# Performance work log

Hardware: AMD Instinct MI355X
Metric: run time of the kernel (lower is better)

Reference implementation:

```python
import jax, jax.numpy as jnp
import numpy as np

LAM = 0.01        # self.lam
K_POINTS = 256    # max diagram points kept for matching


def _diagram0(img):
    """0-dim sublevel-set cubical persistence of a 2D image (V-construction,
    4-connectivity) via Kruskal-style union-find over value-sorted pixels.
    Returns (births, deaths, valid) each of shape [H*W]; essential class gets
    death = max(img). Pairs with zero persistence are masked out (as gudhi does)."""
    H, W = img.shape
    N = H * W
    v = img.reshape(-1)
    order = jnp.argsort(v)          # stable ascending filtration order
    rank = jnp.argsort(order)       # rank[i] = position of pixel i in filtration
    idx = jnp.arange(N)
    rows, cols = idx // W, idx % W
    nbr = jnp.stack([
        jnp.where(rows > 0, idx - W, -1),
        jnp.where(rows < H - 1, idx + W, -1),
        jnp.where(cols > 0, idx - 1, -1),
        jnp.where(cols < W - 1, idx + 1, -1)], axis=1)  # [N,4]

    def find(parent, i):
        # root chase with path halving
        def cond(c):
            p, j = c
            return p[j] != j
        def body(c):
            p, j = c
            pj = p[j]
            return p.at[j].set(p[pj]), pj
        p, r = jax.lax.while_loop(cond, body, (parent, i))
        return p, r

    def step(t, carry):
        parent, death = carry
        p = order[t]  # pixel entering the filtration
        def merge(k, carry2):
            parent, death = carry2
            q = nbr[p, k]
            active = (q >= 0) & (rank[jnp.maximum(q, 0)] < t)
            qs = jnp.where(active, jnp.maximum(q, 0), p)
            parent, rp = find(parent, p)
            parent, rq = find(parent, qs)
            do = active & (rp != rq)
            older = jnp.where(rank[rp] < rank[rq], rp, rq)   # smaller birth survives
            young = jnp.where(rank[rp] < rank[rq], rq, rp)   # younger component dies at v[p]
            parent = parent.at[young].set(jnp.where(do, older, parent[young]))
            death = death.at[young].set(jnp.where(do, p, death[young]))
            return parent, death
        return jax.lax.fori_loop(0, 4, merge, (parent, death))

    parent, death = jax.lax.fori_loop(
        0, N, step, (jnp.arange(N), jnp.full((N,), -1, jnp.int32)))
    births = v
    deaths = jnp.where(death >= 0, v[jnp.maximum(death, 0)], jnp.max(v))
    valid = (deaths - births) > 0
    return births, deaths, valid


def _wdist(b1, d1, m1, b2, d2, m2):
    """2-Wasserstein distance between diagrams, approximated by matching the
    top-K points of each diagram sorted by persistence; unmatched points are
    projected to the diagonal (cost pers^2/2). Final (sum cost)^(1/2) (p=2)."""
    def topk(b, d, m):
        pers = jnp.where(m, d - b, 0.0)
        pk, ix = jax.lax.top_k(pers, K_POINTS)
        return b[ix], d[ix], pk
    b1k, d1k, p1 = topk(b1, d1, m1)
    b2k, d2k, p2 = topk(b2, d2, m2)
    has1, has2 = p1 > 0, p2 > 0
    match = (b1k - b2k) ** 2 + (d1k - d2k) ** 2
    cost = (jnp.where(has1 & has2, match, 0.0)
            + jnp.where(has1 & ~has2, p1 ** 2 * 0.5, 0.0)
            + jnp.where(~has1 & has2, p2 ** 2 * 0.5, 0.0))
    return jnp.sqrt(jnp.sum(cost) + 1e-12)


def _topo_loss(model_output, labels):
    pred = jax.nn.sigmoid(model_output)[:, 0]   # squeeze(dim=1) -> [B,H,W]
    msk = labels[:, 0]
    mn = pred.min(axis=(1, 2), keepdims=True)
    mx = pred.max(axis=(1, 2), keepdims=True)
    pq = jnp.round((pred - mn) / (mx - mn) * 10.0) / 10.0   # 11-level quantization
    mq = jnp.round(msk * 10.0) / 10.0
    bm, dm, vm = jax.vmap(_diagram0)(mq)   # pi_mask
    bp, dp, vp = jax.vmap(_diagram0)(pq)   # pi_pred
    per_sample = jax.vmap(_wdist)(bm, dm, vm, bp, dp, vp)
    return LAM * jnp.sum(per_sample) / pred.shape[0]


def setup_inputs():
    key = jax.random.key(0)
    k1, k2 = jax.random.split(key)
    model_output = jax.random.normal(k1, (4, 1, 128, 128), jnp.float32)
    labels = jax.random.uniform(k2, (4, 1, 128, 128), jnp.float32)
    return {"model_output": model_output, "labels": labels}


def reference(model_output, labels):
    return _topo_loss(model_output, labels)
```

## Files before the change

### kernel.cpp

```cpp
#include <hip/hip_runtime.h>
#include <stdint.h>

#define NPIX 16384
#define IMW 128
#define NIMG 8
#define NLVL 11
#define BIGK 0xFFFFFFFFu
#define IMASK 16383u
#define DONE 0x0D0E0D0Eu

__device__ __forceinline__ unsigned find16(volatile unsigned short* par, unsigned i) {
    unsigned j = par[i];
    while (j != i) {
        unsigned pj = par[j];
        if (pj == j) return j;
        par[i] = (unsigned short)pj;
        i = j; j = pj;
    }
    return i;
}

__device__ __forceinline__ void union16(volatile unsigned short* par, unsigned* par32,
                                        const uint8_t* lvl, unsigned a, unsigned b) {
    unsigned ra = find16(par, a);
    unsigned rb = find16(par, b);
    while (ra != rb) {
        unsigned ka = ((unsigned)lvl[ra] << 14) | ra;
        unsigned kb = ((unsigned)lvl[rb] << 14) | rb;
        unsigned hi = (ka > kb) ? ra : rb;
        unsigned lo = (ka > kb) ? rb : ra;
        unsigned w = hi >> 1, sh = (hi & 1u) * 16u;
        unsigned old32 = ((volatile unsigned*)par32)[w];
        if (((old32 >> sh) & 0xFFFFu) == hi) {
            unsigned new32 = (old32 & ~(0xFFFFu << sh)) | (lo << sh);
            if (atomicCAS(par32 + w, old32, new32) == old32) return;
        }
        ra = find16(par, hi);
        rb = find16(par, lo);
    }
}

__device__ __forceinline__ void flag_release(unsigned* p) {
    __threadfence();
    __hip_atomic_store(p, DONE, __ATOMIC_RELEASE, __HIP_MEMORY_SCOPE_AGENT);
}
__device__ __forceinline__ void flag_acquire(unsigned* p) {
    while (__hip_atomic_load(p, __ATOMIC_ACQUIRE, __HIP_MEMORY_SCOPE_AGENT) != DONE)
        __builtin_amdgcn_s_sleep(2);
}

__global__ __launch_bounds__(1024) void prep_ccl(const float* __restrict__ model_output,
                                                 const float* __restrict__ labels,
                                                 uint8_t* __restrict__ lvl_all,
                                                 int* __restrict__ maxL_all,
                                                 unsigned* __restrict__ argmin_all,
                                                 unsigned* __restrict__ rootmask_all,
                                                 unsigned* __restrict__ flags)
{
    __shared__ __align__(16) unsigned char smem[49152];
    int blk = blockIdx.x;
    int tid = threadIdx.x;
    unsigned lane = tid & 63u;

    if (blk < 8) {
        int img = blk;
        bool ismask = img < 4;
        const float* src = ismask ? (labels + (size_t)img * NPIX)
                                  : (model_output + (size_t)(img - 4) * NPIX);
        uint8_t* lvl = lvl_all + (size_t)img * NPIX;
        unsigned* rm = rootmask_all + (size_t)img * NPIX;
        float* s_f = (float*)smem;
        unsigned* s_u = (unsigned*)(smem + 128);
        float* s_mnmx = (float*)(smem + 256);

        for (int q = tid; q < NPIX / 4; q += 1024)
            ((uint4*)rm)[q] = make_uint4(0, 0, 0, 0);

        float mn = 0.f, mx = 1.f;
        if (!ismask) {
            float lmn = 1e30f, lmx = -1e30f;
            for (int i = tid; i < NPIX; i += 1024) {
                float s = 1.0f / (1.0f + expf(-src[i]));
                lmn = fminf(lmn, s); lmx = fmaxf(lmx, s);
            }
            for (int off = 32; off > 0; off >>= 1) {
                lmn = fminf(lmn, __shfl_down(lmn, off));
                lmx = fmaxf(lmx, __shfl_down(lmx, off));
            }
            int wv = tid >> 6;
            if (lane == 0) { s_f[wv] = lmn; s_f[16 + wv] = lmx; }
            __syncthreads();
            if (tid == 0) {
                float a = s_f[0], c = s_f[16];
                for (int w = 1; w < 16; ++w) { a = fminf(a, s_f[w]); c = fmaxf(c, s_f[16 + w]); }
                s_mnmx[0] = a; s_mnmx[1] = c;
            }
            __syncthreads();
            mn = s_mnmx[0]; mx = s_mnmx[1];
        }
        float denom = mx - mn;
        if (denom <= 0.f) denom = 1.f;

        unsigned lmaxk = 0, bestk = BIGK;
        for (int i = tid; i < NPIX; i += 1024) {
            int L;
            if (ismask) L = (int)rintf(src[i] * 10.0f);
            else {
                float s = 1.0f / (1.0f + expf(-src[i]));
                L = (int)rintf((s - mn) / denom * 10.0f);
            }
            lvl[i] = (uint8_t)L;
            unsigned key = ((unsigned)L << 14) | (unsigned)i;
            lmaxk = max(lmaxk, (unsigned)L);
            bestk = min(bestk, key);
        }
        for (int off = 32; off > 0; off >>= 1) {
            lmaxk = max(lmaxk, (unsigned)__shfl_down((int)lmaxk, off));
            bestk = min(bestk, (unsigned)__shfl_down((int)bestk, off));
        }
        if (lane == 0) { s_u[tid >> 6] = lmaxk; s_u[16 + (tid >> 6)] = bestk; }
        __syncthreads();
        if (tid == 0) {
            unsigned m = s_u[0], b = s_u[16];
            for (int w = 1; w < 16; ++w) { m = max(m, s_u[w]); b = min(b, s_u[16 + w]); }
            maxL_all[img] = (int)m;
            argmin_all[img] = b & IMASK;
            flag_release(&flags[img]);
        }
        return;
    }

    int b = blk - 8;
    int img = b / NLVL, l = b % NLVL;
    int w = tid >> 6;
    uint8_t* s_lvl = (uint8_t*)smem;
    unsigned* s_par32 = (unsigned*)(smem + 16384);
    volatile unsigned short* par = (volatile unsigned short*)s_par32;
    unsigned* rm = rootmask_all + (size_t)img * NPIX;

    if (tid == 0) flag_acquire(&flags[img]);
    __syncthreads();
    int maxL = maxL_all[img];

    if (l >= maxL) {
        if (tid == 0) atomicOr(&rm[argmin_all[img]], 1u << l);
        return;
    }

    ((uint4*)s_lvl)[tid] = ((const uint4*)(lvl_all + (size_t)img * NPIX))[tid];
    __syncthreads();

    unsigned am = 0;
#pragma unroll
    for (int k = 0; k < 16; ++k) {
        int i = (w << 10) + (k << 6) + (int)lane;
        uint8_t Lv = s_lvl[i];
        bool act = (int)Lv <= l;
        if (act) am |= 1u << k;
        unsigned long long m = __ballot(act);
        unsigned key = act ? (((unsigned)Lv << 14) | (unsigned)i) : BIGK;
        unsigned long long lowmask = (1ull << lane) - 1ull;
        unsigned long long zb = (~m) & lowmask;
        int runstart = zb ? (64 - __clzll(zb)) : 0;
        unsigned v = key;
#pragma unroll
        for (int d = 1; d < 64; d <<= 1) {
            unsigned o = __shfl_up(v, d, 64);
            if ((int)lane - d >= runstart) v = min(v, o);
        }
        unsigned long long za = (lane == 63u) ? 0ull : ((~m) >> (lane + 1));
        int runend = za ? ((int)lane + __ffsll((long long)za) - 1) : 63;
        unsigned rmin = __shfl(v, runend, 64);
        par[i] = (unsigned short)(act ? (rmin & IMASK) : (unsigned)i);
    }

    unsigned amL  = (unsigned)__shfl_up((int)am, 1, 64);
    unsigned am63 = (unsigned)__shfl((int)am, 63, 64);

#pragma unroll
    for (int k = 0; k < 16; ++k) {
        if (!((am >> k) & 1u)) continue;
        int i = (w << 10) + (k << 6) + (int)lane;
        if ((k & 1) && lane == 0u && ((am63 >> (k - 1)) & 1u))
            union16(par, s_par32, s_lvl, (unsigned)i, (unsigned)(i - 1));
        if (k >= 2 && ((am >> (k - 2)) & 1u)) {
            bool leftpair = (lane > 0u) && ((amL >> k) & 1u) && ((amL >> (k - 2)) & 1u);
            if (!leftpair)
                union16(par, s_par32, s_lvl, (unsigned)i, (unsigned)(i - IMW));
        }
    }
    __syncthreads();

    if (w >= 1) {
#pragma unroll
        for (int k = 0; k < 2; ++k) {
            if (!((am >> k) & 1u)) continue;
            int i = (w << 10) + (k << 6) + (int)lane;
            if (s_lvl[i - IMW] <= l) {
                int col = (k << 6) + (int)lane;
                bool lact = (lane > 0u) ? (((amL >> k) & 1u) != 0u)
                                        : (k == 1 ? (((am63 >> 0) & 1u) != 0u) : false);
                bool leftpair = (col != 0) && lact && (s_lvl[i - 1 - IMW] <= l);
                if (!leftpair)
                    union16(par, s_par32, s_lvl, (unsigned)i, (unsigned)(i - IMW));
            }
        }
    }
    __syncthreads();

#pragma unroll
    for (int k = 0; k < 16; ++k) {
        if (!((am >> k) & 1u)) continue;
        int i = (w << 10) + (k << 6) + (int)lane;
        if (par[i] == (unsigned short)i) atomicOr(&rm[i], 1u << l);
    }
}

__global__ __launch_bounds__(1024) void death_kernel(const uint8_t* __restrict__ lvl_all,
                                                     const int* __restrict__ maxL_all,
                                                     const unsigned* __restrict__ rootmask_all,
                                                     float* __restrict__ outP,
                                                     float* __restrict__ outB,
                                                     float* __restrict__ outD)
{
    __shared__ uint8_t  s_lvl[NPIX];
    __shared__ uint8_t  s_rank[NPIX];
    __shared__ unsigned long long s_bm[256];
    __shared__ unsigned s_keys[256];
    __shared__ unsigned s_pc[256];
    __shared__ unsigned s_hist[64];
    __shared__ uint8_t  s_rtab[NLVL * NLVL];
    __shared__ unsigned s_ctl[4];

    int img = blockIdx.x;
    int tid = threadIdx.x;
    const uint8_t* lv = lvl_all + (size_t)img * NPIX;
    const unsigned* rmg = rootmask_all + (size_t)img * NPIX;
    int maxL = maxL_all[img];

    ((uint4*)s_lvl)[tid] = ((const uint4*)lv)[tid];
    if (tid < 64) s_hist[tid] = 0;
    if (tid < 256) { s_bm[tid] = 0ull; s_keys[tid] = 0xFFFFFFFFu; }
    if (tid < NLVL * NLVL) {
        int d = tid / NLVL, bb0 = tid % NLVL;
        if (d > bb0) {
            float pers = (float)d / 10.0f - (float)bb0 / 10.0f;
            unsigned rk = 0;
            for (int dd = 1; dd <= 10; ++dd)
                for (int bb = 0; bb < dd; ++bb) {
                    float pp = (float)dd / 10.0f - (float)bb / 10.0f;
                    rk += (pp > pers) ? 1u : 0u;
                }
            s_rtab[d * NLVL + bb0] = (uint8_t)rk;
        }
    }
    __syncthreads();

    for (int i = tid; i < NPIX; i += 1024) {
        uint8_t r = 0xFF;
        int b = s_lvl[i];
        unsigned rmv = rmg[i];
        if ((rmv >> b) & 1u) {
            unsigned inv = (~rmv) >> (b + 1);
            int d = b + 1 + (__ffs(inv) - 1);
            d = min(d, maxL);
            if (d > b) { r = s_rtab[d * NLVL + b]; atomicAdd(&s_hist[r], 1u); }
        }
        s_rank[i] = r;
    }
    __syncthreads();

    if (tid == 0) {
        unsigned cum = 0, rstar = 63, cless = 0;
        for (int r = 0; r < 56; ++r) {
            if (cum + s_hist[r] >= 256u && rstar == 63u) { rstar = r; cless = cum; }
            cum += s_hist[r];
        }
        if (rstar == 63u) cless = cum;
        s_ctl[0] = rstar; s_ctl[1] = cless;
        s_ctl[2] = (rstar == 63u) ? 0u : (256u - cless);
        s_ctl[3] = 0;
    }
    __syncthreads();
    unsigned rstar = s_ctl[0], cless = s_ctl[1], mneed = s_ctl[2];

    for (int i = tid; i < NPIX; i += 1024) {
        unsigned r = s_rank[i];
        if (r == 0xFFu) continue;
        if (r < rstar) {
            unsigned pos = atomicAdd(&s_ctl[3], 1u);
            if (pos < 256u) s_keys[pos] = (r << 14) | (unsigned)i;
        } else if (r == rstar) {
            atomicOr(&s_bm[i >> 6], 1ull << (i & 63));
        }
    }
    __syncthreads();

    for (unsigned kk = 2; kk <= 256; kk <<= 1) {
        for (unsigned j = kk >> 1; j > 0; j >>= 1) {
            if (tid < 256) {
                unsigned i = (unsigned)tid, ixj = i ^ j;
                if (ixj > i) {
                    unsigned x = s_keys[i], y = s_keys[ixj];
                    bool up = ((i & kk) == 0);
                    if ((x > y) == up) { s_keys[i] = y; s_keys[ixj] = x; }
                }
            }
            __syncthreads();
        }
    }

    if (tid < 256) s_pc[tid] = (unsigned)__popcll(s_bm[tid]);
    __syncthreads();
    for (int d = 1; d < 256; d <<= 1) {
        unsigned x = 0;
        if (tid < 256 && tid >= d) x = s_pc[tid - d];
        __syncthreads();
        if (tid < 256 && tid >= d) s_pc[tid] += x;
        __syncthreads();
    }
    for (int i = tid; i < NPIX; i += 1024) {
        if (s_rank[i] != rstar || rstar == 63u) continue;
        if (!((s_bm[i >> 6] >> (i & 63)) & 1ull)) continue;
        unsigned w = i >> 6;
        unsigned order = (w ? s_pc[w - 1] : 0u)
                       + (unsigned)__popcll(s_bm[w] & ((1ull << (i & 63)) - 1ull));
        if (order < mneed) s_keys[cless + order] = (rstar << 14) | (unsigned)i;
    }
    __syncthreads();

    for (int s = tid; s < 256; s += 1024) {
        unsigned key = s_keys[s];
        float p = 0.f, bv = 0.f, dv = 0.f;
        if (key != 0xFFFFFFFFu) {
            unsigned i = key & IMASK;
            int b = s_lvl[i];
            unsigned rmv = rmg[i];
            unsigned inv = (~rmv) >> (b + 1);
            int d = b + 1 + (__ffs(inv) - 1);
            d = min(d, maxL);
            bv = (float)b / 10.0f;
            dv = (float)d / 10.0f;
            p = dv - bv;
        }
        outP[img * 256 + s] = p;
        outB[img * 256 + s] = bv;
        outD[img * 256 + s] = dv;
    }
}

__global__ __launch_bounds__(1024) void wdist_kernel(const float* __restrict__ outP,
                                                     const float* __restrict__ outB,
                                                     const float* __restrict__ outD,
                                                     float* __restrict__ out)
{
    int tid = threadIdx.x;
    int s = tid >> 8;
    int slot = tid & 255;
    int mi = s * 256 + slot;
    int pi = (4 + s) * 256 + slot;
    float p1 = outP[mi], b1 = outB[mi], d1 = outD[mi];
    float p2 = outP[pi], b2 = outB[pi], d2 = outD[pi];
    bool h1 = p1 > 0.f, h2 = p2 > 0.f;
    float cost = 0.f;
    if (h1 && h2)      cost = (b1 - b2) * (b1 - b2) + (d1 - d2) * (d1 - d2);
    else if (h1)       cost = p1 * p1 * 0.5f;
    else if (h2)       cost = p2 * p2 * 0.5f;

    for (int off = 32; off > 0; off >>= 1) cost += __shfl_down(cost, off);
    __shared__ float part[16];
    __shared__ float dist[4];
    int wv = tid >> 6;
    if ((tid & 63) == 0) part[wv] = cost;
    __syncthreads();
    if (tid < 4) {
        float sum = part[tid * 4] + part[tid * 4 + 1] + part[tid * 4 + 2] + part[tid * 4 + 3];
        dist[tid] = sqrtf(sum + 1e-12f);
    }
    __syncthreads();
    if (tid == 0)
        out[0] = 0.01f * (dist[0] + dist[1] + dist[2] + dist[3]) / 4.0f;
}

extern "C" void kernel_launch(void* const* d_in, const int* in_sizes, int n_in,
                              void* d_out, int out_size, void* d_ws, size_t ws_size,
                              hipStream_t stream)
{
    const float* model_output = (const float*)d_in[0];
    const float* labels = (const float*)d_in[1];
    char* ws = (char*)d_ws;
    uint8_t* lvl = (uint8_t*)ws;
    int* maxL = (int*)(ws + 131072);
    unsigned* argmin = (unsigned*)(ws + 131104);
    unsigned* rootmask = (unsigned*)(ws + 131136);
    float* outP = (float*)(ws + 655424);
    float* outB = outP + NIMG * 256;
    float* outD = outB + NIMG * 256;
    unsigned* flags = (unsigned*)(ws + 680000);
    float* out = (float*)d_out;

    prep_ccl<<<96, 1024, 0, stream>>>(model_output, labels, lvl, maxL, argmin,
                                      rootmask, flags);
    death_kernel<<<NIMG, 1024, 0, stream>>>(lvl, maxL, rootmask, outP, outB, outD);
    wdist_kernel<<<1, 1024, 0, stream>>>(outP, outB, outD, out);
}
```

Before: 141.6 us.

## Fuse CCL, death extraction and Wasserstein stages into one flag-synchronized kernel

Merges the three kernel launches into a single 105-block kernel. Blocks take roles by block index: prep, per-level CCL, per-image death/top-K, and the final reduction. Each stage waits on release/acquire flags in global memory instead of a kernel boundary. This removes two launch gaps and their drain/ramp costs, and lets later stages start as soon as their inputs are ready. The cost is spin-waiting blocks. Flags are never reset between calls, so on repeated runs the acquires can pass early and read stale data, which adds a race risk.

```diff
diff --git a/kernel.cpp b/kernel.cpp
--- a/kernel.cpp
+++ b/kernel.cpp
@@ -49,15 +49,19 @@
         __builtin_amdgcn_s_sleep(2);
 }
 
-__global__ __launch_bounds__(1024) void prep_ccl(const float* __restrict__ model_output,
-                                                 const float* __restrict__ labels,
-                                                 uint8_t* __restrict__ lvl_all,
-                                                 int* __restrict__ maxL_all,
-                                                 unsigned* __restrict__ argmin_all,
-                                                 unsigned* __restrict__ rootmask_all,
-                                                 unsigned* __restrict__ flags)
+__global__ __launch_bounds__(1024) void topo_fused(const float* __restrict__ model_output,
+                                                   const float* __restrict__ labels,
+                                                   uint8_t* __restrict__ lvl_all,
+                                                   int* __restrict__ maxL_all,
+                                                   unsigned* __restrict__ argmin_all,
+                                                   unsigned* __restrict__ rootmask_all,
+                                                   float* __restrict__ outP,
+                                                   float* __restrict__ outB,
+                                                   float* __restrict__ outD,
+                                                   unsigned* __restrict__ flags,
+                                                   float* __restrict__ out)
 {
-    __shared__ __align__(16) unsigned char smem[49152];
+    __shared__ __align__(16) unsigned char smem[49664];
     int blk = blockIdx.x;
     int tid = threadIdx.x;
     unsigned lane = tid & 63u;
@@ -130,256 +134,261 @@
         return;
     }
 
-    int b = blk - 8;
-    int img = b / NLVL, l = b % NLVL;
-    int w = tid >> 6;
-    uint8_t* s_lvl = (uint8_t*)smem;
-    unsigned* s_par32 = (unsigned*)(smem + 16384);
-    volatile unsigned short* par = (volatile unsigned short*)s_par32;
-    unsigned* rm = rootmask_all + (size_t)img * NPIX;
-
-    if (tid == 0) flag_acquire(&flags[img]);
-    __syncthreads();
-    int maxL = maxL_all[img];
-
-    if (l >= maxL) {
-        if (tid == 0) atomicOr(&rm[argmin_all[img]], 1u << l);
-        return;
-    }
-
-    ((uint4*)s_lvl)[tid] = ((const uint4*)(lvl_all + (size_t)img * NPIX))[tid];
-    __syncthreads();
-
-    unsigned am = 0;
+    if (blk < 96) {
+        int b = blk - 8;
+        int img = b / NLVL, l = b % NLVL;
+        int w = tid >> 6;
+        uint8_t* s_lvl = (uint8_t*)smem;
+        unsigned* s_par32 = (unsigned*)(smem + 16384);
+        volatile unsigned short* par = (volatile unsigned short*)s_par32;
+        unsigned* rm = rootmask_all + (size_t)img * NPIX;
+
+        if (tid == 0) flag_acquire(&flags[img]);
+        __syncthreads();
+        int maxL = maxL_all[img];
+
+        if (l >= maxL) {
+            if (tid == 0) {
+                atomicOr(&rm[argmin_all[img]], 1u << l);
+                flag_release(&flags[8 + b]);
+            }
+            return;
+        }
+
+        ((uint4*)s_lvl)[tid] = ((const uint4*)(lvl_all + (size_t)img * NPIX))[tid];
+        __syncthreads();
+
+        unsigned am = 0;
 #pragma unroll
-    for (int k = 0; k < 16; ++k) {
-        int i = (w << 10) + (k << 6) + (int)lane;
-        uint8_t Lv = s_lvl[i];
-        bool act = (int)Lv <= l;
-        if (act) am |= 1u << k;
-        unsigned long long m = __ballot(act);
-        unsigned key = act ? (((unsigned)Lv << 14) | (unsigned)i) : BIGK;
-        unsigned long long lowmask = (1ull << lane) - 1ull;
-        unsigned long long zb = (~m) & lowmask;
-        int runstart = zb ? (64 - __clzll(zb)) : 0;
-        unsigned v = key;
+        for (int k = 0; k < 16; ++k) {
+            int i = (w << 10) + (k << 6) + (int)lane;
+            uint8_t Lv = s_lvl[i];
+            bool act = (int)Lv <= l;
+            if (act) am |= 1u << k;
+            unsigned long long m = __ballot(act);
+            unsigned key = act ? (((unsigned)Lv << 14) | (unsigned)i) : BIGK;
+            unsigned long long lowmask = (1ull << lane) - 1ull;
+            unsigned long long zb = (~m) & lowmask;
+            int runstart = zb ? (64 - __clzll(zb)) : 0;
+            unsigned v = key;
 #pragma unroll
-        for (int d = 1; d < 64; d <<= 1) {
-            unsigned o = __shfl_up(v, d, 64);
-            if ((int)lane - d >= runstart) v = min(v, o);
-        }
-        unsigned long long za = (lane == 63u) ? 0ull : ((~m) >> (lane + 1));
-        int runend = za ? ((int)lane + __ffsll((long long)za) - 1) : 63;
-        unsigned rmin = __shfl(v, runend, 64);
-        par[i] = (unsigned short)(act ? (rmin & IMASK) : (unsigned)i);
-    }
-
-    unsigned amL  = (unsigned)__shfl_up((int)am, 1, 64);
-    unsigned am63 = (unsigned)__shfl((int)am, 63, 64);
+            for (int d = 1; d < 64; d <<= 1) {
+                unsigned o = __shfl_up(v, d, 64);
+                if ((int)lane - d >= runstart) v = min(v, o);
+            }
+            unsigned long long za = (lane == 63u) ? 0ull : ((~m) >> (lane + 1));
+            int runend = za ? ((int)lane + __ffsll((long long)za) - 1) : 63;
+            unsigned rmin = __shfl(v, runend, 64);
+            par[i] = (unsigned short)(act ? (rmin & IMASK) : (unsigned)i);
+        }
+
+        unsigned amL  = (unsigned)__shfl_up((int)am, 1, 64);
+        unsigned am63 = (unsigned)__shfl((int)am, 63, 64);
 
 #pragma unroll
-    for (int k = 0; k < 16; ++k) {
-        if (!((am >> k) & 1u)) continue;
-        int i = (w << 10) + (k << 6) + (int)lane;
-        if ((k & 1) && lane == 0u && ((am63 >> (k - 1)) & 1u))
-            union16(par, s_par32, s_lvl, (unsigned)i, (unsigned)(i - 1));
-        if (k >= 2 && ((am >> (k - 2)) & 1u)) {
-            bool leftpair = (lane > 0u) && ((amL >> k) & 1u) && ((amL >> (k - 2)) & 1u);
-            if (!leftpair)
-                union16(par, s_par32, s_lvl, (unsigned)i, (unsigned)(i - IMW));
-        }
-    }
-    __syncthreads();
-
-    if (w >= 1) {
-#pragma unroll
-        for (int k = 0; k < 2; ++k) {
+        for (int k = 0; k < 16; ++k) {
             if (!((am >> k) & 1u)) continue;
             int i = (w << 10) + (k << 6) + (int)lane;
-            if (s_lvl[i - IMW] <= l) {
-                int col = (k << 6) + (int)lane;
-                bool lact = (lane > 0u) ? (((amL >> k) & 1u) != 0u)
-                                        : (k == 1 ? (((am63 >> 0) & 1u) != 0u) : false);
-                bool leftpair = (col != 0) && lact && (s_lvl[i - 1 - IMW] <= l);
+            if ((k & 1) && lane == 0u && ((am63 >> (k - 1)) & 1u))
+                union16(par, s_par32, s_lvl, (unsigned)i, (unsigned)(i - 1));
+            if (k >= 2 && ((am >> (k - 2)) & 1u)) {
+                bool leftpair = (lane > 0u) && ((amL >> k) & 1u) && ((amL >> (k - 2)) & 1u);
                 if (!leftpair)
                     union16(par, s_par32, s_lvl, (unsigned)i, (unsigned)(i - IMW));
             }
         }
-    }
-    __syncthreads();
-
+        __syncthreads();
+
+        if (w >= 1) {
 #pragma unroll
-    for (int k = 0; k < 16; ++k) {
-        if (!((am >> k) & 1u)) continue;
-        int i = (w << 10) + (k << 6) + (int)lane;
-        if (par[i] == (unsigned short)i) atomicOr(&rm[i], 1u << l);
-    }
-}
-
-__global__ __launch_bounds__(1024) void death_kernel(const uint8_t* __restrict__ lvl_all,
-                                                     const int* __restrict__ maxL_all,
-                                                     const unsigned* __restrict__ rootmask_all,
-                                                     float* __restrict__ outP,
-                                                     float* __restrict__ outB,
-                                                     float* __restrict__ outD)
-{
-    __shared__ uint8_t  s_lvl[NPIX];
-    __shared__ uint8_t  s_rank[NPIX];
-    __shared__ unsigned long long s_bm[256];
-    __shared__ unsigned s_keys[256];
-    __shared__ unsigned s_pc[256];
-    __shared__ unsigned s_hist[64];
-    __shared__ uint8_t  s_rtab[NLVL * NLVL];
-    __shared__ unsigned s_ctl[4];
-
-    int img = blockIdx.x;
-    int tid = threadIdx.x;
-    const uint8_t* lv = lvl_all + (size_t)img * NPIX;
-    const unsigned* rmg = rootmask_all + (size_t)img * NPIX;
-    int maxL = maxL_all[img];
-
-    ((uint4*)s_lvl)[tid] = ((const uint4*)lv)[tid];
-    if (tid < 64) s_hist[tid] = 0;
-    if (tid < 256) { s_bm[tid] = 0ull; s_keys[tid] = 0xFFFFFFFFu; }
-    if (tid < NLVL * NLVL) {
-        int d = tid / NLVL, bb0 = tid % NLVL;
-        if (d > bb0) {
-            float pers = (float)d / 10.0f - (float)bb0 / 10.0f;
-            unsigned rk = 0;
-            for (int dd = 1; dd <= 10; ++dd)
-                for (int bb = 0; bb < dd; ++bb) {
-                    float pp = (float)dd / 10.0f - (float)bb / 10.0f;
-                    rk += (pp > pers) ? 1u : 0u;
+            for (int k = 0; k < 2; ++k) {
+                if (!((am >> k) & 1u)) continue;
+                int i = (w << 10) + (k << 6) + (int)lane;
+                if (s_lvl[i - IMW] <= l) {
+                    int col = (k << 6) + (int)lane;
+                    bool lact = (lane > 0u) ? (((amL >> k) & 1u) != 0u)
+                                            : (k == 1 ? (((am63 >> 0) & 1u) != 0u) : false);
+                    bool leftpair = (col != 0) && lact && (s_lvl[i - 1 - IMW] <= l);
+                    if (!leftpair)
+                        union16(par, s_par32, s_lvl, (unsigned)i, (unsigned)(i - IMW));
                 }
-            s_rtab[d * NLVL + bb0] = (uint8_t)rk;
-        }
-    }
-    __syncthreads();
-
-    for (int i = tid; i < NPIX; i += 1024) {
-        uint8_t r = 0xFF;
-        int b = s_lvl[i];
-        unsigned rmv = rmg[i];
-        if ((rmv >> b) & 1u) {
-            unsigned inv = (~rmv) >> (b + 1);
-            int d = b + 1 + (__ffs(inv) - 1);
-            d = min(d, maxL);
-            if (d > b) { r = s_rtab[d * NLVL + b]; atomicAdd(&s_hist[r], 1u); }
-        }
-        s_rank[i] = r;
-    }
-    __syncthreads();
-
-    if (tid == 0) {
-        unsigned cum = 0, rstar = 63, cless = 0;
-        for (int r = 0; r < 56; ++r) {
-            if (cum + s_hist[r] >= 256u && rstar == 63u) { rstar = r; cless = cum; }
-            cum += s_hist[r];
-        }
-        if (rstar == 63u) cless = cum;
-        s_ctl[0] = rstar; s_ctl[1] = cless;
-        s_ctl[2] = (rstar == 63u) ? 0u : (256u - cless);
-        s_ctl[3] = 0;
-    }
-    __syncthreads();
-    unsigned rstar = s_ctl[0], cless = s_ctl[1], mneed = s_ctl[2];
-
-    for (int i = tid; i < NPIX; i += 1024) {
-        unsigned r = s_rank[i];
-        if (r == 0xFFu) continue;
-        if (r < rstar) {
-            unsigned pos = atomicAdd(&s_ctl[3], 1u);
-            if (pos < 256u) s_keys[pos] = (r << 14) | (unsigned)i;
-        } else if (r == rstar) {
-            atomicOr(&s_bm[i >> 6], 1ull << (i & 63));
-        }
-    }
-    __syncthreads();
-
-    for (unsigned kk = 2; kk <= 256; kk <<= 1) {
-        for (unsigned j = kk >> 1; j > 0; j >>= 1) {
-            if (tid < 256) {
-                unsigned i = (unsigned)tid, ixj = i ^ j;
-                if (ixj > i) {
-                    unsigned x = s_keys[i], y = s_keys[ixj];
-                    bool up = ((i & kk) == 0);
-                    if ((x > y) == up) { s_keys[i] = y; s_keys[ixj] = x; }
-                }
-            }
-            __syncthreads();
-        }
-    }
-
-    if (tid < 256) s_pc[tid] = (unsigned)__popcll(s_bm[tid]);
-    __syncthreads();
-    for (int d = 1; d < 256; d <<= 1) {
-        unsigned x = 0;
-        if (tid < 256 && tid >= d) x = s_pc[tid - d];
-        __syncthreads();
-        if (tid < 256 && tid >= d) s_pc[tid] += x;
-        __syncthreads();
-    }
-    for (int i = tid; i < NPIX; i += 1024) {
-        if (s_rank[i] != rstar || rstar == 63u) continue;
-        if (!((s_bm[i >> 6] >> (i & 63)) & 1ull)) continue;
-        unsigned w = i >> 6;
-        unsigned order = (w ? s_pc[w - 1] : 0u)
-                       + (unsigned)__popcll(s_bm[w] & ((1ull << (i & 63)) - 1ull));
-        if (order < mneed) s_keys[cless + order] = (rstar << 14) | (unsigned)i;
-    }
-    __syncthreads();
-
-    for (int s = tid; s < 256; s += 1024) {
-        unsigned key = s_keys[s];
-        float p = 0.f, bv = 0.f, dv = 0.f;
-        if (key != 0xFFFFFFFFu) {
-            unsigned i = key & IMASK;
+            }
+        }
+        __syncthreads();
+
+#pragma unroll
+        for (int k = 0; k < 16; ++k) {
+            if (!((am >> k) & 1u)) continue;
+            int i = (w << 10) + (k << 6) + (int)lane;
+            if (par[i] == (unsigned short)i) atomicOr(&rm[i], 1u << l);
+        }
+        __syncthreads();
+        if (tid == 0) flag_release(&flags[8 + b]);
+        return;
+    }
+
+    if (blk < 104) {
+        int img = blk - 96;
+        uint8_t*  s_lvl  = (uint8_t*)smem;
+        uint8_t*  s_rank = (uint8_t*)(smem + 16384);
+        unsigned long long* s_bm = (unsigned long long*)(smem + 32768);
+        unsigned* s_keys = (unsigned*)(smem + 34816);
+        unsigned* s_pc   = (unsigned*)(smem + 35840);
+        unsigned* s_hist = (unsigned*)(smem + 36864);
+        uint8_t*  s_rtab = (uint8_t*)(smem + 37120);
+        unsigned* s_ctl  = (unsigned*)(smem + 37248);
+
+        if (tid < NLVL) flag_acquire(&flags[8 + img * NLVL + tid]);
+        __syncthreads();
+
+        const uint8_t* lv = lvl_all + (size_t)img * NPIX;
+        const unsigned* rmg = rootmask_all + (size_t)img * NPIX;
+        int maxL = maxL_all[img];
+
+        ((uint4*)s_lvl)[tid] = ((const uint4*)lv)[tid];
+        if (tid < 64) s_hist[tid] = 0;
+        if (tid < 256) { s_bm[tid] = 0ull; s_keys[tid] = 0xFFFFFFFFu; }
+        if (tid < NLVL * NLVL) {
+            int d = tid / NLVL, bb0 = tid % NLVL;
+            if (d > bb0) {
+                float pers = (float)d / 10.0f - (float)bb0 / 10.0f;
+                unsigned rk = 0;
+                for (int dd = 1; dd <= 10; ++dd)
+                    for (int bb = 0; bb < dd; ++bb) {
+                        float pp = (float)dd / 10.0f - (float)bb / 10.0f;
+                        rk += (pp > pers) ? 1u : 0u;
+                    }
+                s_rtab[d * NLVL + bb0] = (uint8_t)rk;
+            }
+        }
+        __syncthreads();
+
+        for (int i = tid; i < NPIX; i += 1024) {
+            uint8_t r = 0xFF;
             int b = s_lvl[i];
             unsigned rmv = rmg[i];
-            unsigned inv = (~rmv) >> (b + 1);
-            int d = b + 1 + (__ffs(inv) - 1);
-            d = min(d, maxL);
-            bv = (float)b / 10.0f;
-            dv = (float)d / 10.0f;
-            p = dv - bv;
-        }
-        outP[img * 256 + s] = p;
-        outB[img * 256 + s] = bv;
-        outD[img * 256 + s] = dv;
-    }
-}
-
-__global__ __launch_bounds__(1024) void wdist_kernel(const float* __restrict__ outP,
-                                                     const float* __restrict__ outB,
-                                                     const float* __restrict__ outD,
-                                                     float* __restrict__ out)
-{
-    int tid = threadIdx.x;
-    int s = tid >> 8;
-    int slot = tid & 255;
-    int mi = s * 256 + slot;
-    int pi = (4 + s) * 256 + slot;
-    float p1 = outP[mi], b1 = outB[mi], d1 = outD[mi];
-    float p2 = outP[pi], b2 = outB[pi], d2 = outD[pi];
-    bool h1 = p1 > 0.f, h2 = p2 > 0.f;
-    float cost = 0.f;
-    if (h1 && h2)      cost = (b1 - b2) * (b1 - b2) + (d1 - d2) * (d1 - d2);
-    else if (h1)       cost = p1 * p1 * 0.5f;
-    else if (h2)       cost = p2 * p2 * 0.5f;
-
-    for (int off = 32; off > 0; off >>= 1) cost += __shfl_down(cost, off);
-    __shared__ float part[16];
-    __shared__ float dist[4];
-    int wv = tid >> 6;
-    if ((tid & 63) == 0) part[wv] = cost;
-    __syncthreads();
-    if (tid < 4) {
-        float sum = part[tid * 4] + part[tid * 4 + 1] + part[tid * 4 + 2] + part[tid * 4 + 3];
-        dist[tid] = sqrtf(sum + 1e-12f);
-    }
-    __syncthreads();
-    if (tid == 0)
-        out[0] = 0.01f * (dist[0] + dist[1] + dist[2] + dist[3]) / 4.0f;
+            if ((rmv >> b) & 1u) {
+                unsigned inv = (~rmv) >> (b + 1);
+                int d = b + 1 + (__ffs(inv) - 1);
+                d = min(d, maxL);
+                if (d > b) { r = s_rtab[d * NLVL + b]; atomicAdd(&s_hist[r], 1u); }
+            }
+            s_rank[i] = r;
+        }
+        __syncthreads();
+
+        if (tid == 0) {
+            unsigned cum = 0, rstar = 63, cless = 0;
+            for (int r = 0; r < 56; ++r) {
+                if (cum + s_hist[r] >= 256u && rstar == 63u) { rstar = r; cless = cum; }
+                cum += s_hist[r];
+            }
+            if (rstar == 63u) cless = cum;
+            s_ctl[0] = rstar; s_ctl[1] = cless;
+            s_ctl[2] = (rstar == 63u) ? 0u : (256u - cless);
+            s_ctl[3] = 0;
+        }
+        __syncthreads();
+        unsigned rstar = s_ctl[0], cless = s_ctl[1], mneed = s_ctl[2];
+
+        for (int i = tid; i < NPIX; i += 1024) {
+            unsigned r = s_rank[i];
+            if (r == 0xFFu) continue;
+            if (r < rstar) {
+                unsigned pos = atomicAdd(&s_ctl[3], 1u);
+                if (pos < 256u) s_keys[pos] = (r << 14) | (unsigned)i;
+            } else if (r == rstar) {
+                atomicOr(&s_bm[i >> 6], 1ull << (i & 63));
+            }
+        }
+        __syncthreads();
+
+        for (unsigned kk = 2; kk <= 256; kk <<= 1) {
+            for (unsigned j = kk >> 1; j > 0; j >>= 1) {
+                if (tid < 256) {
+                    unsigned i = (unsigned)tid, ixj = i ^ j;
+                    if (ixj > i) {
+                        unsigned x = s_keys[i], y = s_keys[ixj];
+                        bool up = ((i & kk) == 0);
+                        if ((x > y) == up) { s_keys[i] = y; s_keys[ixj] = x; }
+                    }
+                }
+                __syncthreads();
+            }
+        }
+
+        if (tid < 256) s_pc[tid] = (unsigned)__popcll(s_bm[tid]);
+        __syncthreads();
+        for (int d = 1; d < 256; d <<= 1) {
+            unsigned x = 0;
+            if (tid < 256 && tid >= d) x = s_pc[tid - d];
+            __syncthreads();
+            if (tid < 256 && tid >= d) s_pc[tid] += x;
+            __syncthreads();
+        }
+        for (int i = tid; i < NPIX; i += 1024) {
+            if (s_rank[i] != rstar || rstar == 63u) continue;
+            if (!((s_bm[i >> 6] >> (i & 63)) & 1ull)) continue;
+            unsigned w = i >> 6;
+            unsigned order = (w ? s_pc[w - 1] : 0u)
+                           + (unsigned)__popcll(s_bm[w] & ((1ull << (i & 63)) - 1ull));
+            if (order < mneed) s_keys[cless + order] = (rstar << 14) | (unsigned)i;
+        }
+        __syncthreads();
+
+        for (int s = tid; s < 256; s += 1024) {
+            unsigned key = s_keys[s];
+            float p = 0.f, bv = 0.f, dv = 0.f;
+            if (key != 0xFFFFFFFFu) {
+                unsigned i = key & IMASK;
+                int b = s_lvl[i];
+                unsigned rmv = rmg[i];
+                unsigned inv = (~rmv) >> (b + 1);
+                int d = b + 1 + (__ffs(inv) - 1);
+                d = min(d, maxL);
+                bv = (float)b / 10.0f;
+                dv = (float)d / 10.0f;
+                p = dv - bv;
+            }
+            outP[img * 256 + s] = p;
+            outB[img * 256 + s] = bv;
+            outD[img * 256 + s] = dv;
+        }
+        __syncthreads();
+        if (tid == 0) flag_release(&flags[96 + img]);
+        return;
+    }
+
+    {
+        if (tid < 8) flag_acquire(&flags[96 + tid]);
+        __syncthreads();
+
+        float* part = (float*)smem;
+        float* dist = (float*)(smem + 64);
+        int s = tid >> 8;
+        int slot = tid & 255;
+        int mi = s * 256 + slot;
+        int pi = (4 + s) * 256 + slot;
+        float p1 = outP[mi], b1 = outB[mi], d1 = outD[mi];
+        float p2 = outP[pi], b2 = outB[pi], d2 = outD[pi];
+        bool h1 = p1 > 0.f, h2 = p2 > 0.f;
+        float cost = 0.f;
+        if (h1 && h2)      cost = (b1 - b2) * (b1 - b2) + (d1 - d2) * (d1 - d2);
+        else if (h1)       cost = p1 * p1 * 0.5f;
+        else if (h2)       cost = p2 * p2 * 0.5f;
+
+        for (int off = 32; off > 0; off >>= 1) cost += __shfl_down(cost, off);
+        int wv = tid >> 6;
+        if (lane == 0u) part[wv] = cost;
+        __syncthreads();
+        if (tid < 4) {
+            float sum = part[tid * 4] + part[tid * 4 + 1] + part[tid * 4 + 2] + part[tid * 4 + 3];
+            dist[tid] = sqrtf(sum + 1e-12f);
+        }
+        __syncthreads();
+        if (tid == 0)
+            out[0] = 0.01f * (dist[0] + dist[1] + dist[2] + dist[3]) / 4.0f;
+    }
 }
 
 extern "C" void kernel_launch(void* const* d_in, const int* in_sizes, int n_in,
@@ -399,8 +408,6 @@
     unsigned* flags = (unsigned*)(ws + 680000);
     float* out = (float*)d_out;
 
-    prep_ccl<<<96, 1024, 0, stream>>>(model_output, labels, lvl, maxL, argmin,
-                                      rootmask, flags);
-    death_kernel<<<NIMG, 1024, 0, stream>>>(lvl, maxL, rootmask, outP, outB, outD);
-    wdist_kernel<<<1, 1024, 0, stream>>>(outP, outB, outD, out);
-}
+    topo_fused<<<105, 1024, 0, stream>>>(model_output, labels, lvl, maxL, argmin,
+                                         rootmask, outP, outB, outD, flags, out);
+}
```

New measurement: 142.5 us. About the same (+0.7%).

## Split prep and CCL kernels, use 32-bit level-packed parent keys in union-find

Applied to the files above, without the earlier changes.

The fused prep+CCL kernel with flag-based inter-block waiting is split into two separate launches, so the CCL blocks no longer spin on acquire flags. The union-find parent array changes from 16-bit indices plus a separate level array to 32-bit keys that pack level and index, so root comparison and CAS work directly on the key without extra level lookups. This costs one extra kernel launch and twice the shared memory for the parent array, and levels are now read from global memory instead of a shared copy.

```diff
diff --git a/kernel.cpp b/kernel.cpp
--- a/kernel.cpp
+++ b/kernel.cpp
@@ -7,139 +7,122 @@
 #define NLVL 11
 #define BIGK 0xFFFFFFFFu
 #define IMASK 16383u
-#define DONE 0x0D0E0D0Eu
-
-__device__ __forceinline__ unsigned find16(volatile unsigned short* par, unsigned i) {
-    unsigned j = par[i];
-    while (j != i) {
-        unsigned pj = par[j];
-        if (pj == j) return j;
-        par[i] = (unsigned short)pj;
-        i = j; j = pj;
-    }
-    return i;
-}
-
-__device__ __forceinline__ void union16(volatile unsigned short* par, unsigned* par32,
-                                        const uint8_t* lvl, unsigned a, unsigned b) {
-    unsigned ra = find16(par, a);
-    unsigned rb = find16(par, b);
-    while (ra != rb) {
-        unsigned ka = ((unsigned)lvl[ra] << 14) | ra;
-        unsigned kb = ((unsigned)lvl[rb] << 14) | rb;
-        unsigned hi = (ka > kb) ? ra : rb;
-        unsigned lo = (ka > kb) ? rb : ra;
-        unsigned w = hi >> 1, sh = (hi & 1u) * 16u;
-        unsigned old32 = ((volatile unsigned*)par32)[w];
-        if (((old32 >> sh) & 0xFFFFu) == hi) {
-            unsigned new32 = (old32 & ~(0xFFFFu << sh)) | (lo << sh);
-            if (atomicCAS(par32 + w, old32, new32) == old32) return;
-        }
-        ra = find16(par, hi);
-        rb = find16(par, lo);
-    }
-}
-
-__device__ __forceinline__ void flag_release(unsigned* p) {
-    __threadfence();
-    __hip_atomic_store(p, DONE, __ATOMIC_RELEASE, __HIP_MEMORY_SCOPE_AGENT);
-}
-__device__ __forceinline__ void flag_acquire(unsigned* p) {
-    while (__hip_atomic_load(p, __ATOMIC_ACQUIRE, __HIP_MEMORY_SCOPE_AGENT) != DONE)
-        __builtin_amdgcn_s_sleep(2);
-}
-
-__global__ __launch_bounds__(1024) void prep_ccl(const float* __restrict__ model_output,
-                                                 const float* __restrict__ labels,
-                                                 uint8_t* __restrict__ lvl_all,
-                                                 int* __restrict__ maxL_all,
-                                                 unsigned* __restrict__ argmin_all,
-                                                 unsigned* __restrict__ rootmask_all,
-                                                 unsigned* __restrict__ flags)
-{
-    __shared__ __align__(16) unsigned char smem[49152];
-    int blk = blockIdx.x;
+
+__device__ __forceinline__ unsigned findk(volatile unsigned* par, unsigned i) {
+    unsigned k = par[i];
+    for (;;) {
+        unsigned j = k & IMASK;
+        unsigned pk = par[j];
+        if (pk == k) return k;
+        par[i] = pk;
+        i = j; k = pk;
+    }
+}
+
+__device__ __forceinline__ void unionk(volatile unsigned* par, unsigned* par32,
+                                       unsigned a, unsigned b) {
+    unsigned ka = findk(par, a);
+    unsigned kb = findk(par, b);
+    while (ka != kb) {
+        unsigned hi = max(ka, kb);
+        unsigned lo = min(ka, kb);
+        unsigned hidx = hi & IMASK;
+        if (atomicCAS(par32 + hidx, hi, lo) == hi) return;
+        ka = findk(par, hidx);
+        kb = findk(par, lo & IMASK);
+    }
+}
+
+__global__ __launch_bounds__(1024) void prep_kernel(const float* __restrict__ model_output,
+                                                    const float* __restrict__ labels,
+                                                    uint8_t* __restrict__ lvl_all,
+                                                    int* __restrict__ maxL_all,
+                                                    unsigned* __restrict__ argmin_all,
+                                                    unsigned* __restrict__ rootmask_all)
+{
+    int img = blockIdx.x;
     int tid = threadIdx.x;
     unsigned lane = tid & 63u;
-
-    if (blk < 8) {
-        int img = blk;
-        bool ismask = img < 4;
-        const float* src = ismask ? (labels + (size_t)img * NPIX)
-                                  : (model_output + (size_t)(img - 4) * NPIX);
-        uint8_t* lvl = lvl_all + (size_t)img * NPIX;
-        unsigned* rm = rootmask_all + (size_t)img * NPIX;
-        float* s_f = (float*)smem;
-        unsigned* s_u = (unsigned*)(smem + 128);
-        float* s_mnmx = (float*)(smem + 256);
-
-        for (int q = tid; q < NPIX / 4; q += 1024)
-            ((uint4*)rm)[q] = make_uint4(0, 0, 0, 0);
-
-        float mn = 0.f, mx = 1.f;
-        if (!ismask) {
-            float lmn = 1e30f, lmx = -1e30f;
-            for (int i = tid; i < NPIX; i += 1024) {
-                float s = 1.0f / (1.0f + expf(-src[i]));
-                lmn = fminf(lmn, s); lmx = fmaxf(lmx, s);
-            }
-            for (int off = 32; off > 0; off >>= 1) {
-                lmn = fminf(lmn, __shfl_down(lmn, off));
-                lmx = fmaxf(lmx, __shfl_down(lmx, off));
-            }
-            int wv = tid >> 6;
-            if (lane == 0) { s_f[wv] = lmn; s_f[16 + wv] = lmx; }
-            __syncthreads();
-            if (tid == 0) {
-                float a = s_f[0], c = s_f[16];
-                for (int w = 1; w < 16; ++w) { a = fminf(a, s_f[w]); c = fmaxf(c, s_f[16 + w]); }
-                s_mnmx[0] = a; s_mnmx[1] = c;
-            }
-            __syncthreads();
-            mn = s_mnmx[0]; mx = s_mnmx[1];
-        }
-        float denom = mx - mn;
-        if (denom <= 0.f) denom = 1.f;
-
-        unsigned lmaxk = 0, bestk = BIGK;
+    bool ismask = img < 4;
+    const float* src = ismask ? (labels + (size_t)img * NPIX)
+                              : (model_output + (size_t)(img - 4) * NPIX);
+    uint8_t* lvl = lvl_all + (size_t)img * NPIX;
+    unsigned* rm = rootmask_all + (size_t)img * NPIX;
+
+    __shared__ float s_f[32];
+    __shared__ unsigned s_u[32];
+    __shared__ float s_mnmx[2];
+
+    for (int q = tid; q < NPIX / 4; q += 1024)
+        ((uint4*)rm)[q] = make_uint4(0, 0, 0, 0);
+
+    float mn = 0.f, mx = 1.f;
+    if (!ismask) {
+        float lmn = 1e30f, lmx = -1e30f;
         for (int i = tid; i < NPIX; i += 1024) {
-            int L;
-            if (ismask) L = (int)rintf(src[i] * 10.0f);
-            else {
-                float s = 1.0f / (1.0f + expf(-src[i]));
-                L = (int)rintf((s - mn) / denom * 10.0f);
-            }
-            lvl[i] = (uint8_t)L;
-            unsigned key = ((unsigned)L << 14) | (unsigned)i;
-            lmaxk = max(lmaxk, (unsigned)L);
-            bestk = min(bestk, key);
+            float s = 1.0f / (1.0f + expf(-src[i]));
+            lmn = fminf(lmn, s); lmx = fmaxf(lmx, s);
         }
         for (int off = 32; off > 0; off >>= 1) {
-            lmaxk = max(lmaxk, (unsigned)__shfl_down((int)lmaxk, off));
-            bestk = min(bestk, (unsigned)__shfl_down((int)bestk, off));
-        }
-        if (lane == 0) { s_u[tid >> 6] = lmaxk; s_u[16 + (tid >> 6)] = bestk; }
+            lmn = fminf(lmn, __shfl_down(lmn, off));
+            lmx = fmaxf(lmx, __shfl_down(lmx, off));
+        }
+        int wv = tid >> 6;
+        if (lane == 0) { s_f[wv] = lmn; s_f[16 + wv] = lmx; }
         __syncthreads();
         if (tid == 0) {
-            unsigned m = s_u[0], b = s_u[16];
-            for (int w = 1; w < 16; ++w) { m = max(m, s_u[w]); b = min(b, s_u[16 + w]); }
-            maxL_all[img] = (int)m;
-            argmin_all[img] = b & IMASK;
-            flag_release(&flags[img]);
-        }
-        return;
-    }
-
-    int b = blk - 8;
+            float a = s_f[0], c = s_f[16];
+            for (int w = 1; w < 16; ++w) { a = fminf(a, s_f[w]); c = fmaxf(c, s_f[16 + w]); }
+            s_mnmx[0] = a; s_mnmx[1] = c;
+        }
+        __syncthreads();
+        mn = s_mnmx[0]; mx = s_mnmx[1];
+    }
+    float denom = mx - mn;
+    if (denom <= 0.f) denom = 1.f;
+
+    unsigned lmaxk = 0, bestk = BIGK;
+    for (int i = tid; i < NPIX; i += 1024) {
+        int L;
+        if (ismask) L = (int)rintf(src[i] * 10.0f);
+        else {
+            float s = 1.0f / (1.0f + expf(-src[i]));
+            L = (int)rintf((s - mn) / denom * 10.0f);
+        }
+        lvl[i] = (uint8_t)L;
+        unsigned key = ((unsigned)L << 14) | (unsigned)i;
+        lmaxk = max(lmaxk, (unsigned)L);
+        bestk = min(bestk, key);
+    }
+    for (int off = 32; off > 0; off >>= 1) {
+        lmaxk = max(lmaxk, (unsigned)__shfl_down((int)lmaxk, off));
+        bestk = min(bestk, (unsigned)__shfl_down((int)bestk, off));
+    }
+    if (lane == 0) { s_u[tid >> 6] = lmaxk; s_u[16 + (tid >> 6)] = bestk; }
+    __syncthreads();
+    if (tid == 0) {
+        unsigned m = s_u[0], b = s_u[16];
+        for (int w = 1; w < 16; ++w) { m = max(m, s_u[w]); b = min(b, s_u[16 + w]); }
+        maxL_all[img] = (int)m;
+        argmin_all[img] = b & IMASK;
+    }
+}
+
+__global__ __launch_bounds__(1024) void ccl_kernel(const uint8_t* __restrict__ lvl_all,
+                                                   const int* __restrict__ maxL_all,
+                                                   const unsigned* __restrict__ argmin_all,
+                                                   unsigned* __restrict__ rootmask_all)
+{
+    __shared__ unsigned s_par[NPIX];
+
+    int b = blockIdx.x;
     int img = b / NLVL, l = b % NLVL;
+    int tid = threadIdx.x;
+    unsigned lane = tid & 63u;
     int w = tid >> 6;
-    uint8_t* s_lvl = (uint8_t*)smem;
-    unsigned* s_par32 = (unsigned*)(smem + 16384);
-    volatile unsigned short* par = (volatile unsigned short*)s_par32;
+    const uint8_t* lv = lvl_all + (size_t)img * NPIX;
     unsigned* rm = rootmask_all + (size_t)img * NPIX;
-
-    if (tid == 0) flag_acquire(&flags[img]);
-    __syncthreads();
+    volatile unsigned* par = s_par;
     int maxL = maxL_all[img];
 
     if (l >= maxL) {
@@ -147,22 +130,20 @@
         return;
     }
 
-    ((uint4*)s_lvl)[tid] = ((const uint4*)(lvl_all + (size_t)img * NPIX))[tid];
-    __syncthreads();
-
     unsigned am = 0;
 #pragma unroll
     for (int k = 0; k < 16; ++k) {
         int i = (w << 10) + (k << 6) + (int)lane;
-        uint8_t Lv = s_lvl[i];
+        unsigned Lv = lv[i];
         bool act = (int)Lv <= l;
         if (act) am |= 1u << k;
+        unsigned key = (Lv << 14) | (unsigned)i;
         unsigned long long m = __ballot(act);
-        unsigned key = act ? (((unsigned)Lv << 14) | (unsigned)i) : BIGK;
+        unsigned kv = act ? key : BIGK;
         unsigned long long lowmask = (1ull << lane) - 1ull;
         unsigned long long zb = (~m) & lowmask;
         int runstart = zb ? (64 - __clzll(zb)) : 0;
-        unsigned v = key;
+        unsigned v = kv;
 #pragma unroll
         for (int d = 1; d < 64; d <<= 1) {
             unsigned o = __shfl_up(v, d, 64);
@@ -171,7 +152,7 @@
         unsigned long long za = (lane == 63u) ? 0ull : ((~m) >> (lane + 1));
         int runend = za ? ((int)lane + __ffsll((long long)za) - 1) : 63;
         unsigned rmin = __shfl(v, runend, 64);
-        par[i] = (unsigned short)(act ? (rmin & IMASK) : (unsigned)i);
+        s_par[i] = act ? rmin : key;
     }
 
     unsigned amL  = (unsigned)__shfl_up((int)am, 1, 64);
@@ -182,11 +163,11 @@
         if (!((am >> k) & 1u)) continue;
         int i = (w << 10) + (k << 6) + (int)lane;
         if ((k & 1) && lane == 0u && ((am63 >> (k - 1)) & 1u))
-            union16(par, s_par32, s_lvl, (unsigned)i, (unsigned)(i - 1));
+            unionk(par, s_par, (unsigned)i, (unsigned)(i - 1));
         if (k >= 2 && ((am >> (k - 2)) & 1u)) {
             bool leftpair = (lane > 0u) && ((amL >> k) & 1u) && ((amL >> (k - 2)) & 1u);
             if (!leftpair)
-                union16(par, s_par32, s_lvl, (unsigned)i, (unsigned)(i - IMW));
+                unionk(par, s_par, (unsigned)i, (unsigned)(i - IMW));
         }
     }
     __syncthreads();
@@ -196,13 +177,13 @@
         for (int k = 0; k < 2; ++k) {
             if (!((am >> k) & 1u)) continue;
             int i = (w << 10) + (k << 6) + (int)lane;
-            if (s_lvl[i - IMW] <= l) {
+            if ((int)(s_par[i - IMW] >> 14) <= l) {
                 int col = (k << 6) + (int)lane;
                 bool lact = (lane > 0u) ? (((amL >> k) & 1u) != 0u)
                                         : (k == 1 ? (((am63 >> 0) & 1u) != 0u) : false);
-                bool leftpair = (col != 0) && lact && (s_lvl[i - 1 - IMW] <= l);
+                bool leftpair = (col != 0) && lact && ((int)(s_par[i - 1 - IMW] >> 14) <= l);
                 if (!leftpair)
-                    union16(par, s_par32, s_lvl, (unsigned)i, (unsigned)(i - IMW));
+                    unionk(par, s_par, (unsigned)i, (unsigned)(i - IMW));
             }
         }
     }
@@ -212,7 +193,7 @@
     for (int k = 0; k < 16; ++k) {
         if (!((am >> k) & 1u)) continue;
         int i = (w << 10) + (k << 6) + (int)lane;
-        if (par[i] == (unsigned short)i) atomicOr(&rm[i], 1u << l);
+        if ((s_par[i] & IMASK) == (unsigned)i) atomicOr(&rm[i], 1u << l);
     }
 }
 
@@ -396,11 +377,10 @@
     float* outP = (float*)(ws + 655424);
     float* outB = outP + NIMG * 256;
     float* outD = outB + NIMG * 256;
-    unsigned* flags = (unsigned*)(ws + 680000);
     float* out = (float*)d_out;
 
-    prep_ccl<<<96, 1024, 0, stream>>>(model_output, labels, lvl, maxL, argmin,
-                                      rootmask, flags);
+    prep_kernel<<<NIMG, 1024, 0, stream>>>(model_output, labels, lvl, maxL, argmin, rootmask);
+    ccl_kernel<<<NIMG * NLVL, 1024, 0, stream>>>(lvl, maxL, argmin, rootmask);
     death_kernel<<<NIMG, 1024, 0, stream>>>(lvl, maxL, rootmask, outP, outB, outD);
     wdist_kernel<<<1, 1024, 0, stream>>>(outP, outB, outD, out);
 }
```

After: 121.9 us. 14.0% less time.
